# Performance work log

Hardware: AMD Instinct MI355X
Metric: run time of the kernel (lower is better)

## Reference

```python
import jax, jax.numpy as jnp
import numpy as np

D_MODEL = 512
D_FFN = 2048
N_LAYERS = 6
VOCAB = 1000
D_STATE = 16
D_CONV = 4
D_INNER = 2 * D_MODEL  # expand=2
DT_RANK = 32           # ceil(d_model/16)
B, LT, LS = 2, 512, 512


def _pos_encoding(length, d_model):
    pos = np.arange(length, dtype=np.float32)[:, None]
    div = np.exp(np.arange(0, d_model, 2, dtype=np.float32) * (-np.log(10000.0) / d_model))
    pe = np.zeros((length, d_model), np.float32)
    pe[:, 0::2] = np.sin(pos * div)
    pe[:, 1::2] = np.cos(pos * div)
    return jnp.asarray(pe)


def _layer_norm(x, g, b, eps=1e-6):
    m = x.mean(-1, keepdims=True)
    v = ((x - m) ** 2).mean(-1, keepdims=True)
    return (x - m) * jax.lax.rsqrt(v + eps) * g + b


def _mamba(x, in_w, conv_w, conv_b, xproj_w, dt_w, dt_b, A_log, Dskip, out_w):
    # x: (b, l, d_model)
    b, l, _ = x.shape
    xz = x @ in_w.T                                   # (b, l, 2*d_inner)
    xc, z = jnp.split(xz, 2, axis=-1)
    # causal depthwise conv over time
    xt = jnp.transpose(xc, (0, 2, 1))                 # (b, d_inner, l)
    xt = jnp.pad(xt, ((0, 0), (0, 0), (D_CONV - 1, 0)))
    xt = jax.lax.conv_general_dilated(
        xt, conv_w, window_strides=(1,), padding='VALID',
        feature_group_count=D_INNER, dimension_numbers=('NCH', 'OIH', 'NCH'))
    xc = jax.nn.silu(jnp.transpose(xt, (0, 2, 1)) + conv_b)  # (b, l, d_inner)
    dbl = xc @ xproj_w.T                              # (b, l, dt_rank + 2*n)
    dt, Bm, Cm = jnp.split(dbl, [DT_RANK, DT_RANK + D_STATE], axis=-1)
    dt = jax.nn.softplus(dt @ dt_w.T + dt_b)          # (b, l, d_inner)
    A = -jnp.exp(A_log)                               # (d_inner, n)

    def step(h, xs):
        dt_t, B_t, C_t, u_t = xs                      # (b,d),(b,n),(b,n),(b,d)
        dA = jnp.exp(dt_t[..., None] * A)             # (b, d, n)
        h = dA * h + (dt_t * u_t)[..., None] * B_t[:, None, :]
        y = jnp.einsum('bdn,bn->bd', h, C_t)
        return h, y

    h0 = jnp.zeros((b, D_INNER, D_STATE), x.dtype)
    xs = (jnp.swapaxes(dt, 0, 1), jnp.swapaxes(Bm, 0, 1),
          jnp.swapaxes(Cm, 0, 1), jnp.swapaxes(xc, 0, 1))
    _, ys = jax.lax.scan(step, h0, xs)                # ys: (l, b, d_inner)
    y = jnp.swapaxes(ys, 0, 1) + xc * Dskip
    y = y * jax.nn.silu(z)
    return y @ out_w.T                                # (b, l, d_model)


def setup_inputs() -> dict:
    key = jax.random.key(0)
    ks = iter(jax.random.split(key, 40))

    def rn(shape, s=0.02):
        return jax.random.normal(next(ks), shape, jnp.float32) * s

    def mamba_params():
        return dict(
            in_w=rn((N_LAYERS, 2 * D_INNER, D_MODEL)),
            conv_w=rn((N_LAYERS, D_INNER, 1, D_CONV), 0.1),
            conv_b=rn((N_LAYERS, D_INNER)),
            xproj=rn((N_LAYERS, DT_RANK + 2 * D_STATE, D_INNER)),
            dtw=rn((N_LAYERS, D_INNER, DT_RANK)),
            dtb=rn((N_LAYERS, D_INNER)),
            Alog=jnp.log(jnp.broadcast_to(jnp.arange(1.0, D_STATE + 1.0, dtype=jnp.float32), (N_LAYERS, D_INNER, D_STATE))),
            D=jnp.ones((N_LAYERS, D_INNER), jnp.float32),
            outw=rn((N_LAYERS, D_MODEL, D_INNER)),
        )

    ps, pc = mamba_params(), mamba_params()
    inp = {
        'src': jax.random.normal(next(ks), (B, LS, D_MODEL), jnp.float32),
        'tgt': jax.random.randint(next(ks), (B, LT), 0, VOCAB),
        'emb': rn((VOCAB, D_MODEL)),
        'in_w_s': ps['in_w'], 'conv_w_s': ps['conv_w'], 'conv_b_s': ps['conv_b'],
        'xproj_s': ps['xproj'], 'dtw_s': ps['dtw'], 'dtb_s': ps['dtb'],
        'Alog_s': ps['Alog'], 'D_s': ps['D'], 'outw_s': ps['outw'],
        'in_w_c': pc['in_w'], 'conv_w_c': pc['conv_w'], 'conv_b_c': pc['conv_b'],
        'xproj_c': pc['xproj'], 'dtw_c': pc['dtw'], 'dtb_c': pc['dtb'],
        'Alog_c': pc['Alog'], 'D_c': pc['D'], 'outw_c': pc['outw'],
        'ffn_w1': rn((N_LAYERS, D_FFN, D_MODEL)),
        'ffn_b1': jnp.zeros((N_LAYERS, D_FFN), jnp.float32),
        'ffn_w2': rn((N_LAYERS, D_MODEL, D_FFN)),
        'ffn_b2': jnp.zeros((N_LAYERS, D_MODEL), jnp.float32),
        'ln_g': jnp.ones((N_LAYERS, 3, D_MODEL), jnp.float32),
        'ln_b': jnp.zeros((N_LAYERS, 3, D_MODEL), jnp.float32),
        'fin_g': jnp.ones((D_MODEL,), jnp.float32),
        'fin_b': jnp.zeros((D_MODEL,), jnp.float32),
    }
    return inp


def reference(src, tgt, emb, in_w_s, conv_w_s, conv_b_s, xproj_s, dtw_s, dtb_s,
              Alog_s, D_s, outw_s, in_w_c, conv_w_c, conv_b_c, xproj_c, dtw_c,
              dtb_c, Alog_c, D_c, outw_c, ffn_w1, ffn_b1, ffn_w2, ffn_b2,
              ln_g, ln_b, fin_g, fin_b):
    # NormalizedEmbedding + sinusoidal positional encoding
    x = emb[tgt] * jnp.sqrt(jnp.asarray(D_MODEL, jnp.float32))
    x = x + _pos_encoding(LT, D_MODEL)[None]
    for i in range(N_LAYERS):
        # self mamba (post-norm, normalize_before=False)
        t2 = _mamba(x, in_w_s[i], conv_w_s[i], conv_b_s[i], xproj_s[i],
                    dtw_s[i], dtb_s[i], Alog_s[i], D_s[i], outw_s[i])
        x = _layer_norm(x + t2, ln_g[i, 0], ln_b[i, 0])
        # cross mamba over concat([memory, tgt]) then take last LT steps
        cat = jnp.concatenate([src, x], axis=1)
        t2 = _mamba(cat, in_w_c[i], conv_w_c[i], conv_b_c[i], xproj_c[i],
                    dtw_c[i], dtb_c[i], Alog_c[i], D_c[i], outw_c[i])[:, -LT:]
        x = _layer_norm(x + t2, ln_g[i, 1], ln_b[i, 1])
        # positionwise FFN
        h = jax.nn.relu(x @ ffn_w1[i].T + ffn_b1[i]) @ ffn_w2[i].T + ffn_b2[i]
        x = _layer_norm(x + h, ln_g[i, 2], ln_b[i, 2])
    return _layer_norm(x, fin_g, fin_b)
```

## Files before the change

### kernel.cpp

```cpp
#include <hip/hip_runtime.h>
#include <math.h>

#define DMODEL 512
#define DINNER 1024
#define DSTATE 16
#define DTRANK 32
#define NLAYERS 6
#define BB 2
#define LT 512
#define LS 512

typedef __attribute__((ext_vector_type(8))) short bf16x8;
typedef __attribute__((ext_vector_type(8))) unsigned short u16x8;
typedef __attribute__((ext_vector_type(4))) float f32x4;

__device__ __forceinline__ unsigned short f2bf(float f) {
  unsigned u = __float_as_uint(f);
  u += 0x7fffu + ((u >> 16) & 1u);
  return (unsigned short)(u >> 16);
}
__device__ __forceinline__ float bf2f(unsigned short u) {
  return __uint_as_float((unsigned)u << 16);
}

template<int EPI>
__device__ __forceinline__ float epi_apply(float acc, float b) {
  if (EPI == 1) { float v = acc + b; return v > 0.f ? v : 0.f; }
  if (EPI == 2) { return acc + b; }
  if (EPI == 3) { float v = acc + b; return fmaxf(v, 0.f) + log1pf(__expf(-fabsf(v))); }
  return acc;
}

__global__ __launch_bounds__(256) void cvt_all_kernel(
    const float* __restrict__ i0, const float* __restrict__ i1,
    const float* __restrict__ i2, const float* __restrict__ i3,
    const float* __restrict__ i4, const float* __restrict__ i5,
    const float* __restrict__ i6, const float* __restrict__ i7,
    const float* __restrict__ i8, const float* __restrict__ i9,
    unsigned short* __restrict__ outbase) {
  int i = blockIdx.x * 256 + threadIdx.x;
  if (i >= 8159232) return;
  const float* in; int off;
  if      (i < 1572864) { in = i0; off = i; }
  else if (i < 3145728) { in = i1; off = i - 1572864; }
  else if (i < 3244032) { in = i2; off = i - 3145728; }
  else if (i < 3342336) { in = i3; off = i - 3244032; }
  else if (i < 3391488) { in = i4; off = i - 3342336; }
  else if (i < 3440640) { in = i5; off = i - 3391488; }
  else if (i < 4227072) { in = i6; off = i - 3440640; }
  else if (i < 5013504) { in = i7; off = i - 4227072; }
  else if (i < 6586368) { in = i8; off = i - 5013504; }
  else                  { in = i9; off = i - 6586368; }
  float4 a = ((const float4*)in)[off];
  ushort4 o = make_ushort4(f2bf(a.x), f2bf(a.y), f2bf(a.z), f2bf(a.w));
  *(ushort4*)&outbase[(size_t)i * 4] = o;
}

__global__ __launch_bounds__(256) void embed_kernel(const int* __restrict__ tgt,
    const float* __restrict__ emb, float* __restrict__ X,
    unsigned short* __restrict__ Xb) {
  int i = blockIdx.x * 256 + threadIdx.x;
  int d = i & (DMODEL - 1);
  int bt = i >> 9;
  int t = bt & (LT - 1);
  int tok = tgt[bt];
  float div = __expf((float)(d & ~1) * (-9.210340371976184f / (float)DMODEL));
  float ang = (float)t * div;
  float pe = (d & 1) ? cosf(ang) : sinf(ang);
  float v = emb[(size_t)tok * DMODEL + d] * 22.627416997969522f + pe;
  X[i] = v;
  Xb[i] = f2bf(v);
}

__global__ __launch_bounds__(256) void catsrc_kernel(const float* __restrict__ src,
    unsigned short* __restrict__ CATb) {
  int i = blockIdx.x * 256 + threadIdx.x;
  int c8 = (i & 63) * 8;
  int r = i >> 6;
  int b = r >> 9, l = r & 511;
  const float* s = src + ((size_t)b * 512 + l) * DMODEL + c8;
  float4 a = *(const float4*)s;
  float4 bq = *(const float4*)(s + 4);
  u16x8 o;
  o[0] = f2bf(a.x); o[1] = f2bf(a.y); o[2] = f2bf(a.z); o[3] = f2bf(a.w);
  o[4] = f2bf(bq.x); o[5] = f2bf(bq.y); o[6] = f2bf(bq.z); o[7] = f2bf(bq.w);
  *(u16x8*)&CATb[((size_t)b * 1024 + l) * DMODEL + c8] = o;
}

template<int BK, int EPI, bool SPLIT, bool OUTB>
__global__ __launch_bounds__(256) void mgemmA(
    const unsigned short* __restrict__ A, const unsigned short* __restrict__ Bw,
    const float* __restrict__ bias, float* __restrict__ C,
    unsigned short* __restrict__ Cb, int M, int N, int K, int lda) {
  constexpr int PAD = BK + 8;
  constexpr int CHA = BK / 32;
  constexpr int CHB = BK / 16;
  __shared__ __align__(16) unsigned short As[64 * PAD];
  __shared__ __align__(16) unsigned short Bs[128 * PAD];
  const int tid = threadIdx.x;
  const int bn = blockIdx.x * 128;
  const int bm = blockIdx.y * 64;
  const int lane = tid & 63;
  const int w = tid >> 6;
  const int wr = (w >> 1) * 32;
  const int wc = (w & 1) * 64;
  const int l15 = lane & 15;
  const int l4 = lane >> 4;
  const int koff = l4 * 8;
  int kcnt = K, kbeg = 0;
  if (SPLIT) { kcnt = K / (int)gridDim.z; kbeg = blockIdx.z * kcnt; }
  const int nt = kcnt / BK;
  f32x4 acc[2][4] = {};

  int arow_[CHA], ak8_[CHA];
  const unsigned short* Ap[CHA];
#pragma unroll
  for (int i = 0; i < CHA; ++i) {
    int f = tid + 256 * i;
    arow_[i] = f / (BK / 8);
    ak8_[i] = (f % (BK / 8)) * 8;
    Ap[i] = A + (size_t)(bm + arow_[i]) * lda + kbeg + ak8_[i];
  }
  int brow_[CHB], bk8_[CHB];
  const unsigned short* Bp[CHB];
#pragma unroll
  for (int i = 0; i < CHB; ++i) {
    int f = tid + 256 * i;
    brow_[i] = f / (BK / 8);
    bk8_[i] = (f % (BK / 8)) * 8;
    Bp[i] = Bw + (size_t)(bn + brow_[i]) * K + kbeg + bk8_[i];
  }

  u16x8 av[CHA], bv[CHB];
#pragma unroll
  for (int i = 0; i < CHA; ++i) av[i] = *(const u16x8*)Ap[i];
#pragma unroll
  for (int i = 0; i < CHB; ++i) bv[i] = *(const u16x8*)Bp[i];

  for (int t = 0; t < nt; ++t) {
    __syncthreads();
#pragma unroll
    for (int i = 0; i < CHA; ++i) *(u16x8*)&As[arow_[i] * PAD + ak8_[i]] = av[i];
#pragma unroll
    for (int i = 0; i < CHB; ++i) *(u16x8*)&Bs[brow_[i] * PAD + bk8_[i]] = bv[i];
    if (t + 1 < nt) {
      int ko = (t + 1) * BK;
#pragma unroll
      for (int i = 0; i < CHA; ++i) av[i] = *(const u16x8*)(Ap[i] + ko);
#pragma unroll
      for (int i = 0; i < CHB; ++i) bv[i] = *(const u16x8*)(Bp[i] + ko);
    }
    __syncthreads();
#pragma unroll
    for (int kk = 0; kk < BK / 32; ++kk) {
      bf16x8 afr[2], bfr[4];
#pragma unroll
      for (int i = 0; i < 2; ++i)
        afr[i] = *(const bf16x8*)&As[(wr + i * 16 + l15) * PAD + kk * 32 + koff];
#pragma unroll
      for (int j = 0; j < 4; ++j)
        bfr[j] = *(const bf16x8*)&Bs[(wc + j * 16 + l15) * PAD + kk * 32 + koff];
#pragma unroll
      for (int fr = 0; fr < 2; ++fr)
#pragma unroll
        for (int fc = 0; fc < 4; ++fc)
          acc[fr][fc] = __builtin_amdgcn_mfma_f32_16x16x32_bf16(
              afr[fr], bfr[fc], acc[fr][fc], 0, 0, 0);
    }
  }

  if (SPLIT) {
    unsigned short* Pz = Cb + (size_t)blockIdx.z * M * N;
#pragma unroll
    for (int fc = 0; fc < 4; ++fc) {
      int col = bn + wc + fc * 16 + l15;
#pragma unroll
      for (int fr = 0; fr < 2; ++fr) {
        int row0 = bm + wr + fr * 16 + l4 * 4;
#pragma unroll
        for (int r = 0; r < 4; ++r)
          Pz[(size_t)(row0 + r) * N + col] = f2bf(acc[fr][fc][r]);
      }
    }
  } else {
#pragma unroll
    for (int fc = 0; fc < 4; ++fc) {
      int col = bn + wc + fc * 16 + l15;
      float bvs = (EPI != 0) ? bias[col] : 0.f;
#pragma unroll
      for (int fr = 0; fr < 2; ++fr) {
        int row0 = bm + wr + fr * 16 + l4 * 4;
#pragma unroll
        for (int r = 0; r < 4; ++r) {
          float v = epi_apply<EPI>(acc[fr][fc][r], bvs);
          if (OUTB) Cb[(size_t)(row0 + r) * N + col] = f2bf(v);
          else      C[(size_t)(row0 + r) * N + col] = v;
        }
      }
    }
  }
}

template<int BK, int EPI, bool SPLIT, bool OUTB>
__global__ __launch_bounds__(256) void mgemm(
    const unsigned short* __restrict__ A, const unsigned short* __restrict__ Bw,
    const float* __restrict__ bias, float* __restrict__ C,
    unsigned short* __restrict__ Cb, int M, int N, int K, int lda) {
  constexpr int PAD = BK + 8;
  constexpr int CH = BK / 32;
  __shared__ __align__(16) unsigned short As[64 * PAD];
  __shared__ __align__(16) unsigned short Bs[64 * PAD];
  const int tid = threadIdx.x;
  const int bn = blockIdx.x * 64;
  const int bm = blockIdx.y * 64;
  const int lane = tid & 63;
  const int w = tid >> 6;
  const int wr = (w >> 1) * 32;
  const int wc = (w & 1) * 32;
  const int l15 = lane & 15;
  const int l4 = lane >> 4;
  const int koff = l4 * 8;
  int kcnt = K, kbeg = 0;
  if (SPLIT) { kcnt = K / (int)gridDim.z; kbeg = blockIdx.z * kcnt; }
  const int nt = kcnt / BK;
  f32x4 acc[2][2] = {};

  int row_[CH], k8_[CH];
  const unsigned short *Ap[CH], *Bp[CH];
#pragma unroll
  for (int i = 0; i < CH; ++i) {
    int f = tid + 256 * i;
    row_[i] = f / (BK / 8);
    k8_[i] = (f % (BK / 8)) * 8;
    Ap[i] = A + (size_t)(bm + row_[i]) * lda + kbeg + k8_[i];
    Bp[i] = Bw + (size_t)(bn + row_[i]) * K + kbeg + k8_[i];
  }

  u16x8 av[CH], bv[CH];
#pragma unroll
  for (int i = 0; i < CH; ++i) { av[i] = *(const u16x8*)Ap[i]; bv[i] = *(const u16x8*)Bp[i]; }

  for (int t = 0; t < nt; ++t) {
    __syncthreads();
#pragma unroll
    for (int i = 0; i < CH; ++i) {
      *(u16x8*)&As[row_[i] * PAD + k8_[i]] = av[i];
      *(u16x8*)&Bs[row_[i] * PAD + k8_[i]] = bv[i];
    }
    if (t + 1 < nt) {
      int ko = (t + 1) * BK;
#pragma unroll
      for (int i = 0; i < CH; ++i) {
        av[i] = *(const u16x8*)(Ap[i] + ko);
        bv[i] = *(const u16x8*)(Bp[i] + ko);
      }
    }
    __syncthreads();
#pragma unroll
    for (int kk = 0; kk < CH; ++kk) {
      bf16x8 afr[2], bfr[2];
#pragma unroll
      for (int i = 0; i < 2; ++i) {
        afr[i] = *(const bf16x8*)&As[(wr + i * 16 + l15) * PAD + kk * 32 + koff];
        bfr[i] = *(const bf16x8*)&Bs[(wc + i * 16 + l15) * PAD + kk * 32 + koff];
      }
#pragma unroll
      for (int fr = 0; fr < 2; ++fr)
#pragma unroll
        for (int fc = 0; fc < 2; ++fc)
          acc[fr][fc] = __builtin_amdgcn_mfma_f32_16x16x32_bf16(
              afr[fr], bfr[fc], acc[fr][fc], 0, 0, 0);
    }
  }

  if (SPLIT) {
    float* Pz = C + (size_t)blockIdx.z * M * N;
#pragma unroll
    for (int fc = 0; fc < 2; ++fc) {
      int col = bn + wc + fc * 16 + l15;
#pragma unroll
      for (int fr = 0; fr < 2; ++fr) {
        int row0 = bm + wr + fr * 16 + l4 * 4;
#pragma unroll
        for (int r = 0; r < 4; ++r)
          Pz[(size_t)(row0 + r) * N + col] = acc[fr][fc][r];
      }
    }
  } else {
#pragma unroll
    for (int fc = 0; fc < 2; ++fc) {
      int col = bn + wc + fc * 16 + l15;
      float bvs = (EPI != 0) ? bias[col] : 0.f;
#pragma unroll
      for (int fr = 0; fr < 2; ++fr) {
        int row0 = bm + wr + fr * 16 + l4 * 4;
#pragma unroll
        for (int r = 0; r < 4; ++r) {
          float v = epi_apply<EPI>(acc[fr][fc][r], bvs);
          if (OUTB) Cb[(size_t)(row0 + r) * N + col] = f2bf(v);
          else      C[(size_t)(row0 + r) * N + col] = v;
        }
      }
    }
  }
}

__global__ __launch_bounds__(256) void conv_silu_kernel(
    const unsigned short* __restrict__ xzb, const float* __restrict__ w,
    const float* __restrict__ bias, unsigned short* __restrict__ outb, int L) {
  int idx = blockIdx.x * 256 + threadIdx.x;
  int d8 = (idx & 127) * 8;
  int bt = idx >> 7;
  int b = bt / L;
  int t = bt - b * L;
  const unsigned short* col = xzb + ((size_t)b * L) * (2 * DINNER) + d8;
  float acc[8];
  float4 wv[8];
#pragma unroll
  for (int j = 0; j < 8; ++j) {
    acc[j] = bias[d8 + j];
    wv[j] = *(const float4*)(w + (size_t)(d8 + j) * 4);
  }
#pragma unroll
  for (int k = 0; k < 4; ++k) {
    int tt = t - 3 + k;
    if (tt >= 0) {
      u16x8 v = *(const u16x8*)(col + (size_t)tt * (2 * DINNER));
      float wk[8] = {
        k == 0 ? wv[0].x : k == 1 ? wv[0].y : k == 2 ? wv[0].z : wv[0].w,
        k == 0 ? wv[1].x : k == 1 ? wv[1].y : k == 2 ? wv[1].z : wv[1].w,
        k == 0 ? wv[2].x : k == 1 ? wv[2].y : k == 2 ? wv[2].z : wv[2].w,
        k == 0 ? wv[3].x : k == 1 ? wv[3].y : k == 2 ? wv[3].z : wv[3].w,
        k == 0 ? wv[4].x : k == 1 ? wv[4].y : k == 2 ? wv[4].z : wv[4].w,
        k == 0 ? wv[5].x : k == 1 ? wv[5].y : k == 2 ? wv[5].z : wv[5].w,
        k == 0 ? wv[6].x : k == 1 ? wv[6].y : k == 2 ? wv[6].z : wv[6].w,
        k == 0 ? wv[7].x : k == 1 ? wv[7].y : k == 2 ? wv[7].z : wv[7].w };
#pragma unroll
      for (int j = 0; j < 8; ++j) acc[j] = fmaf(bf2f(v[j]), wk[j], acc[j]);
    }
  }
  u16x8 o;
#pragma unroll
  for (int j = 0; j < 8; ++j) {
    float sig = 1.f / (1.f + __expf(-acc[j]));
    o[j] = f2bf(acc[j] * sig);
  }
  *(u16x8*)&outb[(size_t)bt * DINNER + d8] = o;
}

__global__ __launch_bounds__(256) void scan_pass1(
    const float* __restrict__ XPP, const unsigned short* __restrict__ u,
    const float* __restrict__ Alog, const float* __restrict__ dtw,
    const float* __restrict__ dtb, float* __restrict__ P, float* __restrict__ S,
    int L, int CL) {
  __shared__ float DBL8[32][64];
  const int tid = threadIdx.x;
  const int d = blockIdx.x * 256 + tid;
  const int b = blockIdx.y;
  const int c = blockIdx.z;
  const int t0 = c * CL;
  if (tid < CL * 8) {
    int t = tid >> 3, j8 = (tid & 7) * 8;
    const float* p = XPP + ((size_t)b * L + t0 + t) * 64 + j8;
    const size_t zs = (size_t)BB * L * 64;
    float s[8] = {0.f, 0.f, 0.f, 0.f, 0.f, 0.f, 0.f, 0.f};
#pragma unroll
    for (int z = 0; z < 8; ++z) {
      float4 a = *(const float4*)(p + z * zs);
      float4 bq = *(const float4*)(p + z * zs + 4);
      s[0] += a.x; s[1] += a.y; s[2] += a.z; s[3] += a.w;
      s[4] += bq.x; s[5] += bq.y; s[6] += bq.z; s[7] += bq.w;
    }
#pragma unroll
    for (int j = 0; j < 8; ++j) DBL8[t][j8 + j] = s[j];
  }
  float A[16];
#pragma unroll
  for (int j = 0; j < 4; ++j) {
    float4 a4 = *(const float4*)(Alog + d * 16 + j * 4);
    A[j * 4 + 0] = -__expf(a4.x); A[j * 4 + 1] = -__expf(a4.y);
    A[j * 4 + 2] = -__expf(a4.z); A[j * 4 + 3] = -__expf(a4.w);
  }
  float wreg[32];
#pragma unroll
  for (int j = 0; j < 8; ++j) {
    float4 w4 = *(const float4*)(dtw + (size_t)d * 32 + j * 4);
    wreg[j*4+0] = w4.x; wreg[j*4+1] = w4.y; wreg[j*4+2] = w4.z; wreg[j*4+3] = w4.w;
  }
  float dtbv = dtb[d];
  float h[16], Pp[16];
#pragma unroll
  for (int n = 0; n < 16; ++n) { h[n] = 0.f; Pp[n] = 1.f; }
  const unsigned short* up = u + ((size_t)b * L + t0) * DINNER + d;
  __syncthreads();
  for (int t = 0; t < CL; ++t) {
    float dtraw = dtbv;
#pragma unroll
    for (int k8 = 0; k8 < 8; ++k8) {
      float4 q = *(const float4*)&DBL8[t][k8 * 4];
      dtraw = fmaf(q.x, wreg[k8*4+0], dtraw);
      dtraw = fmaf(q.y, wreg[k8*4+1], dtraw);
      dtraw = fmaf(q.z, wreg[k8*4+2], dtraw);
      dtraw = fmaf(q.w, wreg[k8*4+3], dtraw);
    }
    float dtv = fmaxf(dtraw, 0.f) + log1pf(__expf(-fabsf(dtraw)));
    float uv = bf2f(up[(size_t)t * DINNER]);
    float du = dtv * uv;
    float Bv[16];
#pragma unroll
    for (int j = 0; j < 4; ++j) {
      float4 b4 = *(const float4*)&DBL8[t][32 + j * 4];
      Bv[j*4+0] = b4.x; Bv[j*4+1] = b4.y; Bv[j*4+2] = b4.z; Bv[j*4+3] = b4.w;
    }
#pragma unroll
    for (int n = 0; n < 16; ++n) {
      float dA = __expf(dtv * A[n]);
      Pp[n] *= dA;
      h[n] = fmaf(dA, h[n], du * Bv[n]);
    }
  }
  size_t base = (size_t)c * 32768 + ((size_t)(b * 1024 + d) << 4);
#pragma unroll
  for (int j = 0; j < 4; ++j) {
    *(float4*)&P[base + j * 4] = make_float4(Pp[j*4], Pp[j*4+1], Pp[j*4+2], Pp[j*4+3]);
    *(float4*)&S[base + j * 4] = make_float4(h[j*4], h[j*4+1], h[j*4+2], h[j*4+3]);
  }
}

__global__ __launch_bounds__(256) void scan_pass2(
    const float* __restrict__ XPP, const unsigned short* __restrict__ u,
    const unsigned short* __restrict__ xzb, const float* __restrict__ Alog,
    const float* __restrict__ dtw, const float* __restrict__ dtb,
    const float* __restrict__ Dsk, const float* __restrict__ P,
    const float* __restrict__ S, unsigned short* __restrict__ ysb,
    int L, int CL, int c0) {
  __shared__ float DBL8[32][64];
  const int tid = threadIdx.x;
  const int d = blockIdx.x * 256 + tid;
  const int b = blockIdx.y;
  const int c = blockIdx.z + c0;
  const int t0 = c * CL;
  if (tid < CL * 8) {
    int t = tid >> 3, j8 = (tid & 7) * 8;
    const float* p = XPP + ((size_t)b * L + t0 + t) * 64 + j8;
    const size_t zs = (size_t)BB * L * 64;
    float s[8] = {0.f, 0.f, 0.f, 0.f, 0.f, 0.f, 0.f, 0.f};
#pragma unroll
    for (int z = 0; z < 8; ++z) {
      float4 a = *(const float4*)(p + z * zs);
      float4 bq = *(const float4*)(p + z * zs + 4);
      s[0] += a.x; s[1] += a.y; s[2] += a.z; s[3] += a.w;
      s[4] += bq.x; s[5] += bq.y; s[6] += bq.z; s[7] += bq.w;
    }
#pragma unroll
    for (int j = 0; j < 8; ++j) DBL8[t][j8 + j] = s[j];
  }
  float A[16];
#pragma unroll
  for (int j = 0; j < 4; ++j) {
    float4 a4 = *(const float4*)(Alog + d * 16 + j * 4);
    A[j * 4 + 0] = -__expf(a4.x); A[j * 4 + 1] = -__expf(a4.y);
    A[j * 4 + 2] = -__expf(a4.z); A[j * 4 + 3] = -__expf(a4.w);
  }
  float wreg[32];
#pragma unroll
  for (int j = 0; j < 8; ++j) {
    float4 w4 = *(const float4*)(dtw + (size_t)d * 32 + j * 4);
    wreg[j*4+0] = w4.x; wreg[j*4+1] = w4.y; wreg[j*4+2] = w4.z; wreg[j*4+3] = w4.w;
  }
  float dtbv = dtb[d];
  float h[16];
#pragma unroll
  for (int n = 0; n < 16; ++n) h[n] = 0.f;
  size_t sbase = (size_t)(b * 1024 + d) << 4;
  for (int cc = 0; cc < c; ++cc) {
    size_t bb = (size_t)cc * 32768 + sbase;
#pragma unroll
    for (int j = 0; j < 4; ++j) {
      float4 p4 = *(const float4*)&P[bb + j * 4];
      float4 s4 = *(const float4*)&S[bb + j * 4];
      h[j*4+0] = fmaf(p4.x, h[j*4+0], s4.x);
      h[j*4+1] = fmaf(p4.y, h[j*4+1], s4.y);
      h[j*4+2] = fmaf(p4.z, h[j*4+2], s4.z);
      h[j*4+3] = fmaf(p4.w, h[j*4+3], s4.w);
    }
  }
  float Dv = Dsk[d];
  const unsigned short* up = u + ((size_t)b * L + t0) * DINNER + d;
  const unsigned short* zp = xzb + ((size_t)b * L + t0) * (2 * DINNER) + DINNER + d;
  unsigned short* yp = ysb + ((size_t)(b * 512) + (t0 - c0 * CL)) * DINNER + d;
  __syncthreads();
  for (int t = 0; t < CL; ++t) {
    float dtraw = dtbv;
#pragma unroll
    for (int k8 = 0; k8 < 8; ++k8) {
      float4 q = *(const float4*)&DBL8[t][k8 * 4];
      dtraw = fmaf(q.x, wreg[k8*4+0], dtraw);
      dtraw = fmaf(q.y, wreg[k8*4+1], dtraw);
      dtraw = fmaf(q.z, wreg[k8*4+2], dtraw);
      dtraw = fmaf(q.w, wreg[k8*4+3], dtraw);
    }
    float dtv = fmaxf(dtraw, 0.f) + log1pf(__expf(-fabsf(dtraw)));
    float uv = bf2f(up[(size_t)t * DINNER]);
    float zv = bf2f(zp[(size_t)t * (2 * DINNER)]);
    float du = dtv * uv;
    float Bv[16], Cv[16];
#pragma unroll
    for (int j = 0; j < 4; ++j) {
      float4 b4 = *(const float4*)&DBL8[t][32 + j * 4];
      float4 c4 = *(const float4*)&DBL8[t][48 + j * 4];
      Bv[j*4+0] = b4.x; Bv[j*4+1] = b4.y; Bv[j*4+2] = b4.z; Bv[j*4+3] = b4.w;
      Cv[j*4+0] = c4.x; Cv[j*4+1] = c4.y; Cv[j*4+2] = c4.z; Cv[j*4+3] = c4.w;
    }
    float y = 0.f;
#pragma unroll
    for (int n = 0; n < 16; ++n) {
      float dA = __expf(dtv * A[n]);
      h[n] = fmaf(dA, h[n], du * Bv[n]);
      y = fmaf(h[n], Cv[n], y);
    }
    float sig = 1.f / (1.f + __expf(-zv));
    yp[(size_t)t * DINNER] = f2bf((y + uv * Dv) * (zv * sig));
  }
}

template<int NZ, int EPI>
__global__ __launch_bounds__(64) void ln_red_kernel(
    const float* __restrict__ res, const unsigned short* __restrict__ Pb,
    const float* __restrict__ bias, const float* __restrict__ g,
    const float* __restrict__ be, float* __restrict__ out,
    unsigned short* __restrict__ outb, int row_scale, int row_off) {
  int r = blockIdx.x;
  int b = r >> 9, t = r & 511;
  int lane = threadIdx.x;
  const float* rp = res + (size_t)r * DMODEL;
  size_t ob = ((size_t)(b * row_scale + row_off + t)) * DMODEL;
  float v[8];
  float s = 0.f, ss = 0.f;
#pragma unroll
  for (int j = 0; j < 8; ++j) {
    int col = lane + j * 64;
    float acc = 0.f;
#pragma unroll
    for (int z = 0; z < NZ; ++z)
      acc += bf2f(Pb[(size_t)z * 524288 + (size_t)r * DMODEL + col]);
    float bv = (EPI != 0) ? bias[col] : 0.f;
    float x = rp[col] + epi_apply<EPI>(acc, bv);
    v[j] = x; s += x; ss += x * x;
  }
#pragma unroll
  for (int o = 32; o > 0; o >>= 1) { s += __shfl_xor(s, o); ss += __shfl_xor(ss, o); }
  float m = s * (1.f / 512.f);
  float var = ss * (1.f / 512.f) - m * m;
  float rs = rsqrtf(var + 1e-6f);
#pragma unroll
  for (int j = 0; j < 8; ++j) {
    int col = lane + j * 64;
    float o2 = (v[j] - m) * rs * g[col] + be[col];
    out[(size_t)r * DMODEL + col] = o2;
    outb[ob + col] = f2bf(o2);
  }
}

__global__ __launch_bounds__(64) void ln_final_kernel(
    const float* __restrict__ res, const float* __restrict__ g,
    const float* __restrict__ be, float* __restrict__ out) {
  int r = blockIdx.x;
  int lane = threadIdx.x;
  const float* rp = res + (size_t)r * DMODEL;
  float v[8];
  float s = 0.f, ss = 0.f;
#pragma unroll
  for (int j = 0; j < 8; ++j) {
    float x = rp[lane + j * 64];
    v[j] = x; s += x; ss += x * x;
  }
#pragma unroll
  for (int o = 32; o > 0; o >>= 1) { s += __shfl_xor(s, o); ss += __shfl_xor(ss, o); }
  float m = s * (1.f / 512.f);
  float var = ss * (1.f / 512.f) - m * m;
  float rs = rsqrtf(var + 1e-6f);
#pragma unroll
  for (int j = 0; j < 8; ++j) {
    int c = lane + j * 64;
    out[(size_t)r * DMODEL + c] = (v[j] - m) * rs * g[c] + be[c];
  }
}

extern "C" void kernel_launch(void* const* d_in, const int* in_sizes, int n_in,
                              void* d_out, int out_size, void* d_ws, size_t ws_size,
                              hipStream_t stream) {
  (void)in_sizes; (void)n_in; (void)out_size; (void)ws_size;
  const float* src      = (const float*)d_in[0];
  const int*   tgt      = (const int*)d_in[1];
  const float* emb      = (const float*)d_in[2];
  const float* in_w_s   = (const float*)d_in[3];
  const float* conv_w_s = (const float*)d_in[4];
  const float* conv_b_s = (const float*)d_in[5];
  const float* xproj_s  = (const float*)d_in[6];
  const float* dtw_s    = (const float*)d_in[7];
  const float* dtb_s    = (const float*)d_in[8];
  const float* Alog_s   = (const float*)d_in[9];
  const float* D_s      = (const float*)d_in[10];
  const float* outw_s   = (const float*)d_in[11];
  const float* in_w_c   = (const float*)d_in[12];
  const float* conv_w_c = (const float*)d_in[13];
  const float* conv_b_c = (const float*)d_in[14];
  const float* xproj_c  = (const float*)d_in[15];
  const float* dtw_c    = (const float*)d_in[16];
  const float* dtb_c    = (const float*)d_in[17];
  const float* Alog_c   = (const float*)d_in[18];
  const float* D_c      = (const float*)d_in[19];
  const float* outw_c   = (const float*)d_in[20];
  const float* ffn_w1   = (const float*)d_in[21];
  const float* ffn_b1   = (const float*)d_in[22];
  const float* ffn_w2   = (const float*)d_in[23];
  const float* ffn_b2   = (const float*)d_in[24];
  const float* ln_g     = (const float*)d_in[25];
  const float* ln_b     = (const float*)d_in[26];
  const float* fin_g    = (const float*)d_in[27];
  const float* fin_b    = (const float*)d_in[28];

  float* ws   = (float*)d_ws;
  float* X    = ws;
  float* XPP  = X + 524288;
  float* SC_P = XPP + 1048576;
  float* SC_S = SC_P + 1048576;
  unsigned short* U = (unsigned short*)(SC_S + 1048576);
  unsigned short* Xb   = U;
  unsigned short* CATb = Xb + 524288;
  unsigned short* XCb  = CATb + 1048576;
  unsigned short* XZb  = XCb + 2097152;
  unsigned short* YSb  = XZb + 4194304;
  unsigned short* XZPb = YSb + 1048576;
  unsigned short* WB   = XZPb + 4194304;
  unsigned short* inwsb = WB;
  unsigned short* inwcb = inwsb + 6291456;
  unsigned short* xpsb  = inwcb + 6291456;
  unsigned short* xpcb  = xpsb + 393216;
  unsigned short* dtwsb = xpcb + 393216;
  unsigned short* dtwcb = dtwsb + 196608;
  unsigned short* owsb  = dtwcb + 196608;
  unsigned short* owcb  = owsb + 3145728;
  unsigned short* f1b   = owcb + 3145728;
  unsigned short* f2b   = f1b + 6291456;

  cvt_all_kernel<<<31872, 256, 0, stream>>>(
      in_w_s, in_w_c, xproj_s, xproj_c, dtw_s, dtw_c, outw_s, outw_c,
      ffn_w1, ffn_w2, WB);
  embed_kernel<<<2048, 256, 0, stream>>>(tgt, emb, X, Xb);
  catsrc_kernel<<<256, 256, 0, stream>>>(src, CATb);

  for (int i = 0; i < NLAYERS; ++i) {
    mgemm<64, 0, false, true><<<dim3(32, 16), 256, 0, stream>>>(
        Xb, inwsb + (size_t)i * 1048576, nullptr, nullptr, XZb, 1024, 2048, 512, 512);
    conv_silu_kernel<<<512, 256, 0, stream>>>(
        XZb, conv_w_s + (size_t)i * 4096, conv_b_s + (size_t)i * 1024, XCb, 512);
    mgemm<64, 0, true, false><<<dim3(1, 16, 8), 256, 0, stream>>>(
        XCb, xpsb + (size_t)i * 65536, nullptr, XPP, nullptr, 1024, 64, 1024, 1024);
    scan_pass1<<<dim3(4, 2, 32), 256, 0, stream>>>(
        XPP, XCb, Alog_s + (size_t)i * 16384, dtw_s + (size_t)i * 32768,
        dtb_s + (size_t)i * 1024, SC_P, SC_S, 512, 16);
    scan_pass2<<<dim3(4, 2, 32), 256, 0, stream>>>(
        XPP, XCb, XZb, Alog_s + (size_t)i * 16384, dtw_s + (size_t)i * 32768,
        dtb_s + (size_t)i * 1024, D_s + (size_t)i * 1024, SC_P, SC_S, YSb, 512, 16, 0);
    mgemmA<64, 0, true, false><<<dim3(4, 16, 8), 256, 0, stream>>>(
        YSb, owsb + (size_t)i * 524288, nullptr, nullptr, XZPb, 1024, 512, 1024, 1024);
    ln_red_kernel<8, 0><<<1024, 64, 0, stream>>>(
        X, XZPb, nullptr, ln_g + (size_t)(i * 3 + 0) * 512,
        ln_b + (size_t)(i * 3 + 0) * 512, X, CATb, 1024, 512);

    mgemmA<64, 0, false, true><<<dim3(16, 32), 256, 0, stream>>>(
        CATb, inwcb + (size_t)i * 1048576, nullptr, nullptr, XZb, 2048, 2048, 512, 512);
    conv_silu_kernel<<<1024, 256, 0, stream>>>(
        XZb, conv_w_c + (size_t)i * 4096, conv_b_c + (size_t)i * 1024, XCb, 1024);
    mgemm<64, 0, true, false><<<dim3(1, 32, 8), 256, 0, stream>>>(
        XCb, xpcb + (size_t)i * 65536, nullptr, XPP, nullptr, 2048, 64, 1024, 1024);
    scan_pass1<<<dim3(4, 2, 32), 256, 0, stream>>>(
        XPP, XCb, Alog_c + (size_t)i * 16384, dtw_c + (size_t)i * 32768,
        dtb_c + (size_t)i * 1024, SC_P, SC_S, 1024, 32);
    scan_pass2<<<dim3(4, 2, 16), 256, 0, stream>>>(
        XPP, XCb, XZb, Alog_c + (size_t)i * 16384, dtw_c + (size_t)i * 32768,
        dtb_c + (size_t)i * 1024, D_c + (size_t)i * 1024, SC_P, SC_S, YSb, 1024, 32, 16);
    mgemmA<64, 0, true, false><<<dim3(4, 16, 8), 256, 0, stream>>>(
        YSb, owcb + (size_t)i * 524288, nullptr, nullptr, XZPb, 1024, 512, 1024, 1024);
    ln_red_kernel<8, 0><<<1024, 64, 0, stream>>>(
        X, XZPb, nullptr, ln_g + (size_t)(i * 3 + 1) * 512,
        ln_b + (size_t)(i * 3 + 1) * 512, X, Xb, 512, 0);

    mgemm<64, 1, false, true><<<dim3(32, 16), 256, 0, stream>>>(
        Xb, f1b + (size_t)i * 1048576, ffn_b1 + (size_t)i * 2048, nullptr, XZb,
        1024, 2048, 512, 512);
    mgemmA<64, 0, true, false><<<dim3(4, 16, 8), 256, 0, stream>>>(
        XZb, f2b + (size_t)i * 1048576, nullptr, nullptr, XZPb, 1024, 512, 2048, 2048);
    ln_red_kernel<8, 2><<<1024, 64, 0, stream>>>(
        X, XZPb, ffn_b2 + (size_t)i * 512, ln_g + (size_t)(i * 3 + 2) * 512,
        ln_b + (size_t)(i * 3 + 2) * 512, X, Xb, 512, 0);
  }

  ln_final_kernel<<<1024, 64, 0, stream>>>(X, fin_g, fin_b, (float*)d_out);
}
```

Measured before the change: 1.135 ms.

## Fuse causal conv+SiLU with x_proj GEMV and merge embed/cat kernels

Replaces the conv_silu kernel and the split-K x_proj MFMA GEMM, which wrote 8 partial slabs, with one kernel. Each block computes conv+SiLU for two timesteps, keeps the fp32 results in LDS and does the 64-wide x_proj as a scalar FMA dot product. Scan kernels now read a single XP row instead of summing 8 partials, and the embedding and src-cast kernels are merged into one launch. This removes two launches per layer plus the partial-sum traffic, at the cost of a non-MFMA projection that rereads the bf16 weights per pair of rows.

```diff
diff --git a/kernel.cpp b/kernel.cpp
--- a/kernel.cpp
+++ b/kernel.cpp
@@ -56,35 +56,35 @@
   *(ushort4*)&outbase[(size_t)i * 4] = o;
 }
 
-__global__ __launch_bounds__(256) void embed_kernel(const int* __restrict__ tgt,
-    const float* __restrict__ emb, float* __restrict__ X,
-    unsigned short* __restrict__ Xb) {
-  int i = blockIdx.x * 256 + threadIdx.x;
-  int d = i & (DMODEL - 1);
-  int bt = i >> 9;
-  int t = bt & (LT - 1);
-  int tok = tgt[bt];
-  float div = __expf((float)(d & ~1) * (-9.210340371976184f / (float)DMODEL));
-  float ang = (float)t * div;
-  float pe = (d & 1) ? cosf(ang) : sinf(ang);
-  float v = emb[(size_t)tok * DMODEL + d] * 22.627416997969522f + pe;
-  X[i] = v;
-  Xb[i] = f2bf(v);
-}
-
-__global__ __launch_bounds__(256) void catsrc_kernel(const float* __restrict__ src,
+__global__ __launch_bounds__(256) void embed_cat_kernel(const int* __restrict__ tgt,
+    const float* __restrict__ emb, const float* __restrict__ src,
+    float* __restrict__ X, unsigned short* __restrict__ Xb,
     unsigned short* __restrict__ CATb) {
-  int i = blockIdx.x * 256 + threadIdx.x;
-  int c8 = (i & 63) * 8;
-  int r = i >> 6;
-  int b = r >> 9, l = r & 511;
-  const float* s = src + ((size_t)b * 512 + l) * DMODEL + c8;
-  float4 a = *(const float4*)s;
-  float4 bq = *(const float4*)(s + 4);
-  u16x8 o;
-  o[0] = f2bf(a.x); o[1] = f2bf(a.y); o[2] = f2bf(a.z); o[3] = f2bf(a.w);
-  o[4] = f2bf(bq.x); o[5] = f2bf(bq.y); o[6] = f2bf(bq.z); o[7] = f2bf(bq.w);
-  *(u16x8*)&CATb[((size_t)b * 1024 + l) * DMODEL + c8] = o;
+  if (blockIdx.x < 2048) {
+    int i = blockIdx.x * 256 + threadIdx.x;
+    int d = i & (DMODEL - 1);
+    int bt = i >> 9;
+    int t = bt & (LT - 1);
+    int tok = tgt[bt];
+    float div = __expf((float)(d & ~1) * (-9.210340371976184f / (float)DMODEL));
+    float ang = (float)t * div;
+    float pe = (d & 1) ? cosf(ang) : sinf(ang);
+    float v = emb[(size_t)tok * DMODEL + d] * 22.627416997969522f + pe;
+    X[i] = v;
+    Xb[i] = f2bf(v);
+  } else {
+    int i = (blockIdx.x - 2048) * 256 + threadIdx.x;
+    int c8 = (i & 63) * 8;
+    int r = i >> 6;
+    int b = r >> 9, l = r & 511;
+    const float* s = src + ((size_t)b * 512 + l) * DMODEL + c8;
+    float4 a = *(const float4*)s;
+    float4 bq = *(const float4*)(s + 4);
+    u16x8 o;
+    o[0] = f2bf(a.x); o[1] = f2bf(a.y); o[2] = f2bf(a.z); o[3] = f2bf(a.w);
+    o[4] = f2bf(bq.x); o[5] = f2bf(bq.y); o[6] = f2bf(bq.z); o[7] = f2bf(bq.w);
+    *(u16x8*)&CATb[((size_t)b * 1024 + l) * DMODEL + c8] = o;
+  }
 }
 
 template<int BK, int EPI, bool SPLIT, bool OUTB>
@@ -305,51 +305,85 @@
   }
 }
 
-__global__ __launch_bounds__(256) void conv_silu_kernel(
+__global__ __launch_bounds__(256) void conv_xproj_kernel(
     const unsigned short* __restrict__ xzb, const float* __restrict__ w,
-    const float* __restrict__ bias, unsigned short* __restrict__ outb, int L) {
-  int idx = blockIdx.x * 256 + threadIdx.x;
-  int d8 = (idx & 127) * 8;
-  int bt = idx >> 7;
-  int b = bt / L;
-  int t = bt - b * L;
-  const unsigned short* col = xzb + ((size_t)b * L) * (2 * DINNER) + d8;
-  float acc[8];
-  float4 wv[8];
-#pragma unroll
-  for (int j = 0; j < 8; ++j) {
-    acc[j] = bias[d8 + j];
-    wv[j] = *(const float4*)(w + (size_t)(d8 + j) * 4);
-  }
-#pragma unroll
-  for (int k = 0; k < 4; ++k) {
-    int tt = t - 3 + k;
-    if (tt >= 0) {
-      u16x8 v = *(const u16x8*)(col + (size_t)tt * (2 * DINNER));
-      float wk[8] = {
-        k == 0 ? wv[0].x : k == 1 ? wv[0].y : k == 2 ? wv[0].z : wv[0].w,
-        k == 0 ? wv[1].x : k == 1 ? wv[1].y : k == 2 ? wv[1].z : wv[1].w,
-        k == 0 ? wv[2].x : k == 1 ? wv[2].y : k == 2 ? wv[2].z : wv[2].w,
-        k == 0 ? wv[3].x : k == 1 ? wv[3].y : k == 2 ? wv[3].z : wv[3].w,
-        k == 0 ? wv[4].x : k == 1 ? wv[4].y : k == 2 ? wv[4].z : wv[4].w,
-        k == 0 ? wv[5].x : k == 1 ? wv[5].y : k == 2 ? wv[5].z : wv[5].w,
-        k == 0 ? wv[6].x : k == 1 ? wv[6].y : k == 2 ? wv[6].z : wv[6].w,
-        k == 0 ? wv[7].x : k == 1 ? wv[7].y : k == 2 ? wv[7].z : wv[7].w };
-#pragma unroll
-      for (int j = 0; j < 8; ++j) acc[j] = fmaf(bf2f(v[j]), wk[j], acc[j]);
-    }
-  }
-  u16x8 o;
-#pragma unroll
-  for (int j = 0; j < 8; ++j) {
-    float sig = 1.f / (1.f + __expf(-acc[j]));
-    o[j] = f2bf(acc[j] * sig);
-  }
-  *(u16x8*)&outb[(size_t)bt * DINNER + d8] = o;
+    const float* __restrict__ bias, const unsigned short* __restrict__ xpw,
+    unsigned short* __restrict__ outb, float* __restrict__ XP, int L) {
+  __shared__ float XCf[2][1024];
+  const int tid = threadIdx.x;
+  const int grow0 = blockIdx.x * 2;
+  const int b = grow0 / L;
+  const int t0 = grow0 - b * L;
+  {
+    int r = tid >> 7;
+    int d8 = (tid & 127) * 8;
+    int t = t0 + r;
+    const unsigned short* col = xzb + ((size_t)b * L) * (2 * DINNER) + d8;
+    float acc[8];
+    float4 wv[8];
+#pragma unroll
+    for (int j = 0; j < 8; ++j) {
+      acc[j] = bias[d8 + j];
+      wv[j] = *(const float4*)(w + (size_t)(d8 + j) * 4);
+    }
+#pragma unroll
+    for (int k = 0; k < 4; ++k) {
+      int tt = t - 3 + k;
+      if (tt >= 0) {
+        u16x8 v = *(const u16x8*)(col + (size_t)tt * (2 * DINNER));
+        float wk[8] = {
+          k == 0 ? wv[0].x : k == 1 ? wv[0].y : k == 2 ? wv[0].z : wv[0].w,
+          k == 0 ? wv[1].x : k == 1 ? wv[1].y : k == 2 ? wv[1].z : wv[1].w,
+          k == 0 ? wv[2].x : k == 1 ? wv[2].y : k == 2 ? wv[2].z : wv[2].w,
+          k == 0 ? wv[3].x : k == 1 ? wv[3].y : k == 2 ? wv[3].z : wv[3].w,
+          k == 0 ? wv[4].x : k == 1 ? wv[4].y : k == 2 ? wv[4].z : wv[4].w,
+          k == 0 ? wv[5].x : k == 1 ? wv[5].y : k == 2 ? wv[5].z : wv[5].w,
+          k == 0 ? wv[6].x : k == 1 ? wv[6].y : k == 2 ? wv[6].z : wv[6].w,
+          k == 0 ? wv[7].x : k == 1 ? wv[7].y : k == 2 ? wv[7].z : wv[7].w };
+#pragma unroll
+        for (int j = 0; j < 8; ++j) acc[j] = fmaf(bf2f(v[j]), wk[j], acc[j]);
+      }
+    }
+    u16x8 o;
+#pragma unroll
+    for (int j = 0; j < 8; ++j) {
+      float sig = 1.f / (1.f + __expf(-acc[j]));
+      float xv = acc[j] * sig;
+      o[j] = f2bf(xv);
+      XCf[r][d8 + j] = xv;
+    }
+    *(u16x8*)&outb[(size_t)(b * L + t) * DINNER + d8] = o;
+  }
+  __syncthreads();
+  int oid = tid >> 1, half = tid & 1;
+  int r = oid >> 6, n = oid & 63;
+  const unsigned short* wrow = xpw + (size_t)n * 1024 + half * 512;
+  const float* xr = &XCf[r][half * 512];
+  float a0 = 0.f, a1 = 0.f, a2 = 0.f, a3 = 0.f;
+  for (int k8 = 0; k8 < 64; k8 += 4) {
+    u16x8 w0 = *(const u16x8*)(wrow + (k8 + 0) * 8);
+    u16x8 w1 = *(const u16x8*)(wrow + (k8 + 1) * 8);
+    u16x8 w2 = *(const u16x8*)(wrow + (k8 + 2) * 8);
+    u16x8 w3 = *(const u16x8*)(wrow + (k8 + 3) * 8);
+    const float* x0 = xr + (k8 + 0) * 8;
+    const float* x1 = xr + (k8 + 1) * 8;
+    const float* x2 = xr + (k8 + 2) * 8;
+    const float* x3 = xr + (k8 + 3) * 8;
+#pragma unroll
+    for (int j = 0; j < 8; ++j) {
+      a0 = fmaf(x0[j], bf2f(w0[j]), a0);
+      a1 = fmaf(x1[j], bf2f(w1[j]), a1);
+      a2 = fmaf(x2[j], bf2f(w2[j]), a2);
+      a3 = fmaf(x3[j], bf2f(w3[j]), a3);
+    }
+  }
+  float acc = (a0 + a1) + (a2 + a3);
+  acc += __shfl_xor(acc, 1);
+  if (!half) XP[(size_t)(grow0 + r) * 64 + n] = acc;
 }
 
 __global__ __launch_bounds__(256) void scan_pass1(
-    const float* __restrict__ XPP, const unsigned short* __restrict__ u,
+    const float* __restrict__ XP, const unsigned short* __restrict__ u,
     const float* __restrict__ Alog, const float* __restrict__ dtw,
     const float* __restrict__ dtb, float* __restrict__ P, float* __restrict__ S,
     int L, int CL) {
@@ -361,18 +395,13 @@
   const int t0 = c * CL;
   if (tid < CL * 8) {
     int t = tid >> 3, j8 = (tid & 7) * 8;
-    const float* p = XPP + ((size_t)b * L + t0 + t) * 64 + j8;
-    const size_t zs = (size_t)BB * L * 64;
-    float s[8] = {0.f, 0.f, 0.f, 0.f, 0.f, 0.f, 0.f, 0.f};
-#pragma unroll
-    for (int z = 0; z < 8; ++z) {
-      float4 a = *(const float4*)(p + z * zs);
-      float4 bq = *(const float4*)(p + z * zs + 4);
-      s[0] += a.x; s[1] += a.y; s[2] += a.z; s[3] += a.w;
-      s[4] += bq.x; s[5] += bq.y; s[6] += bq.z; s[7] += bq.w;
-    }
-#pragma unroll
-    for (int j = 0; j < 8; ++j) DBL8[t][j8 + j] = s[j];
+    const float* p = XP + ((size_t)b * L + t0 + t) * 64 + j8;
+    float4 a = *(const float4*)p;
+    float4 bq = *(const float4*)(p + 4);
+    DBL8[t][j8 + 0] = a.x; DBL8[t][j8 + 1] = a.y;
+    DBL8[t][j8 + 2] = a.z; DBL8[t][j8 + 3] = a.w;
+    DBL8[t][j8 + 4] = bq.x; DBL8[t][j8 + 5] = bq.y;
+    DBL8[t][j8 + 6] = bq.z; DBL8[t][j8 + 7] = bq.w;
   }
   float A[16];
 #pragma unroll
@@ -428,7 +457,7 @@
 }
 
 __global__ __launch_bounds__(256) void scan_pass2(
-    const float* __restrict__ XPP, const unsigned short* __restrict__ u,
+    const float* __restrict__ XP, const unsigned short* __restrict__ u,
     const unsigned short* __restrict__ xzb, const float* __restrict__ Alog,
     const float* __restrict__ dtw, const float* __restrict__ dtb,
     const float* __restrict__ Dsk, const float* __restrict__ P,
@@ -442,18 +471,13 @@
   const int t0 = c * CL;
   if (tid < CL * 8) {
     int t = tid >> 3, j8 = (tid & 7) * 8;
-    const float* p = XPP + ((size_t)b * L + t0 + t) * 64 + j8;
-    const size_t zs = (size_t)BB * L * 64;
-    float s[8] = {0.f, 0.f, 0.f, 0.f, 0.f, 0.f, 0.f, 0.f};
-#pragma unroll
-    for (int z = 0; z < 8; ++z) {
-      float4 a = *(const float4*)(p + z * zs);
-      float4 bq = *(const float4*)(p + z * zs + 4);
-      s[0] += a.x; s[1] += a.y; s[2] += a.z; s[3] += a.w;
-      s[4] += bq.x; s[5] += bq.y; s[6] += bq.z; s[7] += bq.w;
-    }
-#pragma unroll
-    for (int j = 0; j < 8; ++j) DBL8[t][j8 + j] = s[j];
+    const float* p = XP + ((size_t)b * L + t0 + t) * 64 + j8;
+    float4 a = *(const float4*)p;
+    float4 bq = *(const float4*)(p + 4);
+    DBL8[t][j8 + 0] = a.x; DBL8[t][j8 + 1] = a.y;
+    DBL8[t][j8 + 2] = a.z; DBL8[t][j8 + 3] = a.w;
+    DBL8[t][j8 + 4] = bq.x; DBL8[t][j8 + 5] = bq.y;
+    DBL8[t][j8 + 6] = bq.z; DBL8[t][j8 + 7] = bq.w;
   }
   float A[16];
 #pragma unroll
@@ -623,8 +647,8 @@
 
   float* ws   = (float*)d_ws;
   float* X    = ws;
-  float* XPP  = X + 524288;
-  float* SC_P = XPP + 1048576;
+  float* XP   = X + 524288;
+  float* SC_P = XP + 131072;
   float* SC_S = SC_P + 1048576;
   unsigned short* U = (unsigned short*)(SC_S + 1048576);
   unsigned short* Xb   = U;
@@ -648,21 +672,19 @@
   cvt_all_kernel<<<31872, 256, 0, stream>>>(
       in_w_s, in_w_c, xproj_s, xproj_c, dtw_s, dtw_c, outw_s, outw_c,
       ffn_w1, ffn_w2, WB);
-  embed_kernel<<<2048, 256, 0, stream>>>(tgt, emb, X, Xb);
-  catsrc_kernel<<<256, 256, 0, stream>>>(src, CATb);
+  embed_cat_kernel<<<2304, 256, 0, stream>>>(tgt, emb, src, X, Xb, CATb);
 
   for (int i = 0; i < NLAYERS; ++i) {
     mgemm<64, 0, false, true><<<dim3(32, 16), 256, 0, stream>>>(
         Xb, inwsb + (size_t)i * 1048576, nullptr, nullptr, XZb, 1024, 2048, 512, 512);
-    conv_silu_kernel<<<512, 256, 0, stream>>>(
-        XZb, conv_w_s + (size_t)i * 4096, conv_b_s + (size_t)i * 1024, XCb, 512);
-    mgemm<64, 0, true, false><<<dim3(1, 16, 8), 256, 0, stream>>>(
-        XCb, xpsb + (size_t)i * 65536, nullptr, XPP, nullptr, 1024, 64, 1024, 1024);
+    conv_xproj_kernel<<<512, 256, 0, stream>>>(
+        XZb, conv_w_s + (size_t)i * 4096, conv_b_s + (size_t)i * 1024,
+        xpsb + (size_t)i * 65536, XCb, XP, 512);
     scan_pass1<<<dim3(4, 2, 32), 256, 0, stream>>>(
-        XPP, XCb, Alog_s + (size_t)i * 16384, dtw_s + (size_t)i * 32768,
+        XP, XCb, Alog_s + (size_t)i * 16384, dtw_s + (size_t)i * 32768,
         dtb_s + (size_t)i * 1024, SC_P, SC_S, 512, 16);
     scan_pass2<<<dim3(4, 2, 32), 256, 0, stream>>>(
-        XPP, XCb, XZb, Alog_s + (size_t)i * 16384, dtw_s + (size_t)i * 32768,
+        XP, XCb, XZb, Alog_s + (size_t)i * 16384, dtw_s + (size_t)i * 32768,
         dtb_s + (size_t)i * 1024, D_s + (size_t)i * 1024, SC_P, SC_S, YSb, 512, 16, 0);
     mgemmA<64, 0, true, false><<<dim3(4, 16, 8), 256, 0, stream>>>(
         YSb, owsb + (size_t)i * 524288, nullptr, nullptr, XZPb, 1024, 512, 1024, 1024);
@@ -672,15 +694,14 @@
 
     mgemmA<64, 0, false, true><<<dim3(16, 32), 256, 0, stream>>>(
         CATb, inwcb + (size_t)i * 1048576, nullptr, nullptr, XZb, 2048, 2048, 512, 512);
-    conv_silu_kernel<<<1024, 256, 0, stream>>>(
-        XZb, conv_w_c + (size_t)i * 4096, conv_b_c + (size_t)i * 1024, XCb, 1024);
-    mgemm<64, 0, true, false><<<dim3(1, 32, 8), 256, 0, stream>>>(
-        XCb, xpcb + (size_t)i * 65536, nullptr, XPP, nullptr, 2048, 64, 1024, 1024);
+    conv_xproj_kernel<<<1024, 256, 0, stream>>>(
+        XZb, conv_w_c + (size_t)i * 4096, conv_b_c + (size_t)i * 1024,
+        xpcb + (size_t)i * 65536, XCb, XP, 1024);
     scan_pass1<<<dim3(4, 2, 32), 256, 0, stream>>>(
-        XPP, XCb, Alog_c + (size_t)i * 16384, dtw_c + (size_t)i * 32768,
+        XP, XCb, Alog_c + (size_t)i * 16384, dtw_c + (size_t)i * 32768,
         dtb_c + (size_t)i * 1024, SC_P, SC_S, 1024, 32);
     scan_pass2<<<dim3(4, 2, 16), 256, 0, stream>>>(
-        XPP, XCb, XZb, Alog_c + (size_t)i * 16384, dtw_c + (size_t)i * 32768,
+        XP, XCb, XZb, Alog_c + (size_t)i * 16384, dtw_c + (size_t)i * 32768,
         dtb_c + (size_t)i * 1024, D_c + (size_t)i * 1024, SC_P, SC_S, YSb, 1024, 32, 16);
     mgemmA<64, 0, true, false><<<dim3(4, 16, 8), 256, 0, stream>>>(
         YSb, owcb + (size_t)i * 524288, nullptr, nullptr, XZPb, 1024, 512, 1024, 1024);
```

Measured after the change: 1.317 ms. 1.16x slower.
